# Optimization experiments

Measured on AMD Instinct MI355X. Metric: run time of the kernel, lower is better.

## Reference

```python
import jax, jax.numpy as jnp
import numpy as np


def setup_inputs() -> dict:
    key = jax.random.key(0)
    k1, k2, k3, k4 = jax.random.split(key, 4)
    B, T, C, H = 8, 2048, 1024, 64
    x = jax.random.normal(k1, (B, T, C), dtype=jnp.float32)
    Wq = jax.random.normal(k2, (C, H), dtype=jnp.float32) * (C ** -0.5)
    Wk = jax.random.normal(k3, (C, H), dtype=jnp.float32) * (C ** -0.5)
    Wv = jax.random.normal(k4, (C, H), dtype=jnp.float32) * (C ** -0.5)
    return {"x": x, "Wq": Wq, "Wk": Wk, "Wv": Wv}


def reference(x, Wq, Wk, Wv):
    # x: [B,T,C]; Wq/Wk/Wv: [C,H] (nn.Linear bias=False => x @ W)
    B, T, C = x.shape
    H = Wq.shape[-1]
    q = jnp.einsum('btc,ch->bth', x, Wq)
    k = jnp.einsum('btc,ch->bth', x, Wk)
    v = jnp.einsum('btc,ch->bth', x, Wv)
    scale = H ** -0.5
    att = jnp.einsum('bqh,bkh->bqk', q, k) * scale  # [B,T,T]
    causal = jnp.tril(jnp.ones((T, T), dtype=bool))
    att = jnp.where(causal, att, -jnp.inf)
    att = jax.nn.softmax(att, axis=-1)
    out = jnp.einsum('bqk,bkh->bqh', att, v)  # [B,T,H]
    return out
```

## Files before the change

kernel.cpp:

```cpp
#include <hip/hip_runtime.h>
#include <hip/hip_bf16.h>
#include <math.h>

#define BB 8
#define TT 2048
#define CC 1024
#define HH 64
#define BT (BB * TT)

typedef __attribute__((ext_vector_type(8))) short short8;
typedef __attribute__((ext_vector_type(4))) float floatx4;

static __device__ inline ushort f2bf(float f) {
    __hip_bfloat16 h = __float2bfloat16(f);
    return *reinterpret_cast<ushort*>(&h);
}
static __device__ inline unsigned int f2bf2(float lo, float hi) {
    __hip_bfloat162 h = __float22bfloat162_rn(make_float2(lo, hi));
    return *reinterpret_cast<unsigned int*>(&h);
}
static __device__ inline float bf2f(ushort u) {
    union { unsigned int i; float f; } c;
    c.i = ((unsigned int)u) << 16;
    return c.f;
}
static __device__ inline void gl_lds16(const ushort* g, ushort* l) {
    __builtin_amdgcn_global_load_lds(
        (const __attribute__((address_space(1))) unsigned int*)g,
        (__attribute__((address_space(3))) unsigned int*)l,
        16, 0, 0);
}

__global__ __launch_bounds__(256) void wprep_kernel(
    const float* __restrict__ Wq, const float* __restrict__ Wk,
    const float* __restrict__ Wv, ushort* __restrict__ WbT)
{
    __shared__ float ws_[128 * 65];
    const int m  = blockIdx.x >> 3;
    const int kb = (blockIdx.x & 7) * 128;
    const float* W = (m == 0) ? Wq : (m == 1) ? Wk : Wv;
    const int t  = threadIdx.x;
    const int lr = t >> 4, lc = (t & 15) * 4;
    #pragma unroll
    for (int i = 0; i < 8; ++i) {
        const int row = lr + i * 16;
        float4 v = *(const float4*)&W[(size_t)(kb + row) * HH + lc];
        ws_[row * 65 + lc + 0] = v.x; ws_[row * 65 + lc + 1] = v.y;
        ws_[row * 65 + lc + 2] = v.z; ws_[row * 65 + lc + 3] = v.w;
    }
    __syncthreads();
    const int n = t & 63, kseg = t >> 6;
    union { ushort s[32]; uint4 q[4]; } u;
    #pragma unroll
    for (int j = 0; j < 32; ++j)
        u.s[j] = f2bf(ws_[(kseg * 32 + j) * 65 + n]);
    ushort* dst = &WbT[(size_t)(m * 64 + n) * 1024 + kb + kseg * 32];
    #pragma unroll
    for (int i = 0; i < 4; ++i) *(uint4*)&dst[i * 8] = u.q[i];
}

__global__ __launch_bounds__(256) void qkv_kernel(
    const float* __restrict__ x, const ushort* __restrict__ WbT,
    ushort* __restrict__ qb, ushort* __restrict__ kbS, ushort* __restrict__ vS)
{
    __shared__ ushort As[2][256 * 8];

    const int row0 = blockIdx.x * 32;
    const int t    = threadIdx.x;
    const int w    = t >> 6;
    const int lane = t & 63;
    const int l16  = lane & 15;
    const int quad = lane >> 4;
    const int ct0  = w * 3;

    const int srow = t >> 3, sseg = t & 7;
    const int slot = (((sseg >> 2) * 2 + (srow >> 4)) * 16 + (srow & 15)) * 4 + (sseg & 3);
    const float* xsrc = &x[(size_t)(row0 + srow) * CC + sseg * 8];

    floatx4 acc[2][3];
    #pragma unroll
    for (int mt = 0; mt < 2; ++mt)
        #pragma unroll
        for (int c = 0; c < 3; ++c) acc[mt][c] = (floatx4){0.f, 0.f, 0.f, 0.f};

    float4 xa = *(const float4*)&xsrc[0];
    float4 xb = *(const float4*)&xsrc[4];

    short8 bfr[2][3];
    #pragma unroll
    for (int p = 0; p < 2; ++p)
        #pragma unroll
        for (int c = 0; c < 3; ++c)
            bfr[p][c] = *(const short8*)&WbT[(size_t)((ct0 + c) * 16 + l16) * 1024
                                             + p * 32 + quad * 8];

    #pragma unroll 2
    for (int it = 0; it < 16; ++it) {
        uint4 uq;
        uq.x = f2bf2(xa.x, xa.y); uq.y = f2bf2(xa.z, xa.w);
        uq.z = f2bf2(xb.x, xb.y); uq.w = f2bf2(xb.z, xb.w);
        *(uint4*)&As[it & 1][slot * 8] = uq;
        __syncthreads();

        if (it < 15) {
            xa = *(const float4*)&xsrc[(it + 1) * 64 + 0];
            xb = *(const float4*)&xsrc[(it + 1) * 64 + 4];
        }
        short8 bnx[2][3];
        if (it < 15) {
            const int kn = (it + 1) * 64;
            #pragma unroll
            for (int p = 0; p < 2; ++p)
                #pragma unroll
                for (int c = 0; c < 3; ++c)
                    bnx[p][c] = *(const short8*)&WbT[(size_t)((ct0 + c) * 16 + l16) * 1024
                                                     + kn + p * 32 + quad * 8];
        }

        #pragma unroll
        for (int p = 0; p < 2; ++p) {
            short8 a0 = *(const short8*)&As[it & 1][(size_t)((p * 2 + 0) * 64 + l16 * 4 + quad) * 8];
            short8 a1 = *(const short8*)&As[it & 1][(size_t)((p * 2 + 1) * 64 + l16 * 4 + quad) * 8];
            #pragma unroll
            for (int c = 0; c < 3; ++c) {
                acc[0][c] = __builtin_amdgcn_mfma_f32_16x16x32_bf16(a0, bfr[p][c], acc[0][c], 0, 0, 0);
                acc[1][c] = __builtin_amdgcn_mfma_f32_16x16x32_bf16(a1, bfr[p][c], acc[1][c], 0, 0, 0);
            }
        }
        #pragma unroll
        for (int p = 0; p < 2; ++p)
            #pragma unroll
            for (int c = 0; c < 3; ++c)
                bfr[p][c] = bnx[p][c];
    }

    const int half = (row0 >> 5) & 1;
    const size_t tile = (size_t)(row0 >> 6) * 4096;
    #pragma unroll
    for (int c = 0; c < 3; ++c) {
        const int ct    = ct0 + c;
        const int mtype = ct >> 2;
        const int n0    = (ct & 3) * 16;
        #pragma unroll
        for (int mt = 0; mt < 2; ++mt) {
            const int row = row0 + mt * 16 + quad * 4;
            if (mtype == 0) {
                #pragma unroll
                for (int reg = 0; reg < 4; ++reg)
                    qb[(size_t)(row + reg) * HH + n0 + l16] = f2bf(acc[mt][c][reg] * 0.125f);
            } else if (mtype == 1) {
                const int cP    = half * 2 + mt;
                const int pP    = (ct & 3) >> 1;
                const int quadP = ((ct & 3) * 2 + (l16 >> 3)) & 3;
                const int jP    = l16 & 7;
                const int ub    = (cP * 2 + pP) * 64 + quadP * 16;
                #pragma unroll
                for (int reg = 0; reg < 4; ++reg)
                    kbS[tile + (size_t)(ub + quad * 4 + reg) * 8 + jP] = f2bf(acc[mt][c][reg]);
            } else {
                const int cp2 = (ct & 3) * 2 + half;
                #pragma unroll
                for (int reg = 0; reg < 4; ++reg) {
                    const int rq    = quad * 4 + reg;
                    const int quadP = mt * 2 + (rq >> 3);
                    vS[tile + (size_t)(cp2 * 64 + quadP * 16 + l16) * 8 + (rq & 7)] = f2bf(acc[mt][c][reg]);
                }
            }
        }
    }
}

__global__ __launch_bounds__(256) void attn_kernel(
    const ushort* __restrict__ qb, const ushort* __restrict__ kbS,
    const ushort* __restrict__ vS, ushort* __restrict__ Opart,
    float* __restrict__ ml)
{
    __shared__ __align__(16) ushort Kb[2][4096];
    __shared__ __align__(16) ushort Vb[2][4096];
    __shared__ __align__(16) ushort P[4][16 * 72];

    const int t    = threadIdx.x;
    const int w    = t >> 6;
    const int lane = t & 63;
    const int l16  = lane & 15;
    const int quad = lane >> 4;

    const int b   = blockIdx.x & 7;
    const int idx = blockIdx.x >> 3;
    int qt, part, np;
    if (idx < 32)      { qt = 31 - (idx >> 2); part = idx & 3; np = 4; }
    else if (idx < 56) { const int u = idx - 32; const int g = u / 3;
                         qt = 23 - g; part = u - g * 3; np = 3; }
    else if (idx < 72) { const int u = idx - 56; qt = 15 - (u >> 1); part = u & 1; np = 2; }
    else               { qt = 7 - (idx - 72); part = 0; np = 1; }
    const int ntiles = qt + 1;
    const int ktb = (part * ntiles) / np;
    const int kte = ((part + 1) * ntiles) / np;

    const ushort* ktile0 = kbS + (size_t)(b * 32) * 4096;
    const ushort* vtile0 = vS  + (size_t)(b * 32) * 4096;

    short8 qf[2];
    {
        const ushort* qrow = qb + ((size_t)b * TT + qt * 64 + w * 16) * HH;
        qf[0] = *(const short8*)&qrow[l16 * HH + quad * 8];
        qf[1] = *(const short8*)&qrow[l16 * HH + 32 + quad * 8];
    }
    short8 ones;
    #pragma unroll
    for (int i = 0; i < 8; ++i) ones[i] = (short)0x3F80;

    floatx4 o[4], osum;
    #pragma unroll
    for (int c = 0; c < 4; ++c) o[c] = (floatx4){0.f, 0.f, 0.f, 0.f};
    osum = (floatx4){0.f, 0.f, 0.f, 0.f};

    {
        const ushort* gk = ktile0 + (size_t)ktb * 4096 + w * 1024 + lane * 8;
        const ushort* gv = vtile0 + (size_t)ktb * 4096 + w * 1024 + lane * 8;
        gl_lds16(gk,       &Kb[0][w * 1024]);
        gl_lds16(gk + 512, &Kb[0][w * 1024 + 512]);
        gl_lds16(gv,       &Vb[0][w * 1024]);
        gl_lds16(gv + 512, &Vb[0][w * 1024 + 512]);
    }

    ushort* Pw = &P[w][0];

    for (int kt = ktb; kt < kte; ++kt) {
        const int cur = (kt - ktb) & 1;
        __syncthreads();

        if (kt + 1 < kte) {
            const int nxt = cur ^ 1;
            const ushort* gk = ktile0 + (size_t)(kt + 1) * 4096 + w * 1024 + lane * 8;
            const ushort* gv = vtile0 + (size_t)(kt + 1) * 4096 + w * 1024 + lane * 8;
            gl_lds16(gk,       &Kb[nxt][w * 1024]);
            gl_lds16(gk + 512, &Kb[nxt][w * 1024 + 512]);
            gl_lds16(gv,       &Vb[nxt][w * 1024]);
            gl_lds16(gv + 512, &Vb[nxt][w * 1024 + 512]);
        }

        short8 kf[4][2], vf[4][2];
        #pragma unroll
        for (int c = 0; c < 4; ++c)
            #pragma unroll
            for (int p = 0; p < 2; ++p) {
                kf[c][p] = *(const short8*)&Kb[cur][(size_t)(((c * 2 + p) * 64) + lane) * 8];
                vf[c][p] = *(const short8*)&Vb[cur][(size_t)(((c * 2 + p) * 64) + lane) * 8];
            }

        floatx4 s[4];
        #pragma unroll
        for (int c = 0; c < 4; ++c) s[c] = (floatx4){0.f, 0.f, 0.f, 0.f};
        #pragma unroll
        for (int c = 0; c < 4; ++c)
            #pragma unroll
            for (int p = 0; p < 2; ++p)
                s[c] = __builtin_amdgcn_mfma_f32_16x16x32_bf16(qf[p], kf[c][p], s[c], 0, 0, 0);

        if (kt == ntiles - 1) {
            const int qrow0 = qt * 64 + w * 16 + quad * 4;
            const int key0  = kt * 64;
            #pragma unroll
            for (int c = 0; c < 4; ++c)
                #pragma unroll
                for (int reg = 0; reg < 4; ++reg)
                    if (key0 + c * 16 + l16 > qrow0 + reg) s[c][reg] = -1e30f;
        }

        #pragma unroll
        for (int c = 0; c < 4; ++c)
            #pragma unroll
            for (int reg = 0; reg < 4; ++reg)
                Pw[(quad * 4 + reg) * 72 + c * 16 + l16] = f2bf(__expf(s[c][reg]));

        short8 pf[2];
        pf[0] = *(const short8*)&Pw[l16 * 72 + quad * 8];
        pf[1] = *(const short8*)&Pw[l16 * 72 + 32 + quad * 8];

        #pragma unroll
        for (int p = 0; p < 2; ++p) {
            #pragma unroll
            for (int c = 0; c < 4; ++c)
                o[c] = __builtin_amdgcn_mfma_f32_16x16x32_bf16(pf[p], vf[c][p], o[c], 0, 0, 0);
            osum = __builtin_amdgcn_mfma_f32_16x16x32_bf16(pf[p], ones, osum, 0, 0, 0);
        }
    }

    const size_t ub = (size_t)blockIdx.x * 4096;
    #pragma unroll
    for (int c = 0; c < 4; ++c)
        #pragma unroll
        for (int reg = 0; reg < 4; ++reg)
            Opart[ub + (w * 16 + quad * 4 + reg) * 64 + c * 16 + l16] = f2bf(o[c][reg]);
    if (l16 == 0) {
        #pragma unroll
        for (int reg = 0; reg < 4; ++reg)
            ml[(size_t)blockIdx.x * 64 + w * 16 + quad * 4 + reg] = osum[reg];
    }
}

__global__ __launch_bounds__(256) void merge_kernel(
    const ushort* __restrict__ Opart, const float* __restrict__ ml,
    float* __restrict__ out)
{
    const int t    = threadIdx.x;
    const int gw   = blockIdx.x * 4 + (t >> 6);
    const int lane = t & 63;
    const int b    = gw >> 8;
    const int v    = gw & 255;
    const int qt   = v >> 3;
    const int oct  = v & 7;

    int base, np;
    if (qt >= 24)      { base = (31 - qt) * 4;      np = 4; }
    else if (qt >= 16) { base = 32 + (23 - qt) * 3; np = 3; }
    else if (qt >= 8)  { base = 56 + (15 - qt) * 2; np = 2; }
    else               { base = 72 + (7 - qt);      np = 1; }

    float* obase = out + ((size_t)b * TT + qt * 64) * HH;

    #pragma unroll 2
    for (int row = oct * 8; row < oct * 8 + 8; ++row) {
        float den = 0.f, acc = 0.f;
        for (int p = 0; p < np; ++p) {
            const int unit = (base + p) * 8 + b;
            den += ml[(size_t)unit * 64 + row];
            acc += bf2f(Opart[(size_t)unit * 4096 + row * 64 + lane]);
        }
        obase[(size_t)row * HH + lane] = acc / den;
    }
}

extern "C" void kernel_launch(void* const* d_in, const int* in_sizes, int n_in,
                              void* d_out, int out_size, void* d_ws, size_t ws_size,
                              hipStream_t stream)
{
    (void)in_sizes; (void)n_in; (void)out_size; (void)ws_size;
    const float* x  = (const float*)d_in[0];
    const float* Wq = (const float*)d_in[1];
    const float* Wk = (const float*)d_in[2];
    const float* Wv = (const float*)d_in[3];
    float* outp = (float*)d_out;

    char* base = (char*)d_ws;
    ushort* WbT   = (ushort*)(base);
    ushort* qbuf  = (ushort*)(base + 393216);
    ushort* kbS   = qbuf + (size_t)BT * HH;
    ushort* vSb   = kbS + (size_t)BT * HH;
    ushort* Opart = vSb + (size_t)BT * HH;
    float*  ml    = (float*)((char*)Opart + (size_t)640 * 4096 * 2);

    wprep_kernel<<<dim3(24),  256, 0, stream>>>(Wq, Wk, Wv, WbT);
    qkv_kernel  <<<dim3(512), 256, 0, stream>>>(x, WbT, qbuf, kbS, vSb);
    attn_kernel <<<dim3(640), 256, 0, stream>>>(qbuf, kbS, vSb, Opart, ml);
    merge_kernel<<<dim3(512), 256, 0, stream>>>(Opart, ml, outp);
}
```

Baseline: 145.7 us.

## Split weight prep finer, prefetch x two tiles ahead, vectorize merge

Three separate changes. The weight-prep kernel now uses 48 blocks of 64 rows instead of 24 blocks of 128, to spread the small transpose over more CUs. The QKV projection keeps two register sets of x loads and fetches x two iterations ahead instead of one, to hide global load latency better at the cost of more registers. The merge kernel now reads four bf16 values and writes a float4 per lane, and multiplies by a reciprocal instead of dividing per element, which cuts the number of memory instructions.

```diff
diff --git a/kernel.cpp b/kernel.cpp
--- a/kernel.cpp
+++ b/kernel.cpp
@@ -35,14 +35,14 @@
     const float* __restrict__ Wq, const float* __restrict__ Wk,
     const float* __restrict__ Wv, ushort* __restrict__ WbT)
 {
-    __shared__ float ws_[128 * 65];
-    const int m  = blockIdx.x >> 3;
-    const int kb = (blockIdx.x & 7) * 128;
+    __shared__ float ws_[64 * 65];
+    const int m  = blockIdx.x >> 4;
+    const int kb = (blockIdx.x & 15) * 64;
     const float* W = (m == 0) ? Wq : (m == 1) ? Wk : Wv;
     const int t  = threadIdx.x;
     const int lr = t >> 4, lc = (t & 15) * 4;
     #pragma unroll
-    for (int i = 0; i < 8; ++i) {
+    for (int i = 0; i < 4; ++i) {
         const int row = lr + i * 16;
         float4 v = *(const float4*)&W[(size_t)(kb + row) * HH + lc];
         ws_[row * 65 + lc + 0] = v.x; ws_[row * 65 + lc + 1] = v.y;
@@ -50,13 +50,13 @@
     }
     __syncthreads();
     const int n = t & 63, kseg = t >> 6;
-    union { ushort s[32]; uint4 q[4]; } u;
-    #pragma unroll
-    for (int j = 0; j < 32; ++j)
-        u.s[j] = f2bf(ws_[(kseg * 32 + j) * 65 + n]);
-    ushort* dst = &WbT[(size_t)(m * 64 + n) * 1024 + kb + kseg * 32];
-    #pragma unroll
-    for (int i = 0; i < 4; ++i) *(uint4*)&dst[i * 8] = u.q[i];
+    union { ushort s[16]; uint4 q[2]; } u;
+    #pragma unroll
+    for (int j = 0; j < 16; ++j)
+        u.s[j] = f2bf(ws_[(kseg * 16 + j) * 65 + n]);
+    ushort* dst = &WbT[(size_t)(m * 64 + n) * 1024 + kb + kseg * 16];
+    *(uint4*)&dst[0] = u.q[0];
+    *(uint4*)&dst[8] = u.q[1];
 }
 
 __global__ __launch_bounds__(256) void qkv_kernel(
@@ -83,8 +83,10 @@
         #pragma unroll
         for (int c = 0; c < 3; ++c) acc[mt][c] = (floatx4){0.f, 0.f, 0.f, 0.f};
 
-    float4 xa = *(const float4*)&xsrc[0];
-    float4 xb = *(const float4*)&xsrc[4];
+    float4 xa0 = *(const float4*)&xsrc[0];
+    float4 xb0 = *(const float4*)&xsrc[4];
+    float4 xa1 = *(const float4*)&xsrc[64];
+    float4 xb1 = *(const float4*)&xsrc[68];
 
     short8 bfr[2][3];
     #pragma unroll
@@ -94,17 +96,16 @@
             bfr[p][c] = *(const short8*)&WbT[(size_t)((ct0 + c) * 16 + l16) * 1024
                                              + p * 32 + quad * 8];
 
-    #pragma unroll 2
-    for (int it = 0; it < 16; ++it) {
+    auto body = [&](int it, float4& xa, float4& xb) {
         uint4 uq;
         uq.x = f2bf2(xa.x, xa.y); uq.y = f2bf2(xa.z, xa.w);
         uq.z = f2bf2(xb.x, xb.y); uq.w = f2bf2(xb.z, xb.w);
         *(uint4*)&As[it & 1][slot * 8] = uq;
         __syncthreads();
 
-        if (it < 15) {
-            xa = *(const float4*)&xsrc[(it + 1) * 64 + 0];
-            xb = *(const float4*)&xsrc[(it + 1) * 64 + 4];
+        if (it + 2 < 16) {
+            xa = *(const float4*)&xsrc[(it + 2) * 64 + 0];
+            xb = *(const float4*)&xsrc[(it + 2) * 64 + 4];
         }
         short8 bnx[2][3];
         if (it < 15) {
@@ -132,6 +133,11 @@
             #pragma unroll
             for (int c = 0; c < 3; ++c)
                 bfr[p][c] = bnx[p][c];
+    };
+
+    for (int it2 = 0; it2 < 16; it2 += 2) {
+        body(it2 + 0, xa0, xb0);
+        body(it2 + 1, xa1, xb1);
     }
 
     const int half = (row0 >> 5) & 1;
@@ -318,17 +324,25 @@
     else if (qt >= 8)  { base = 56 + (15 - qt) * 2; np = 2; }
     else               { base = 72 + (7 - qt);      np = 1; }
 
+    const int r4 = lane >> 4;
+    const int cs = (lane & 15) * 4;
     float* obase = out + ((size_t)b * TT + qt * 64) * HH;
 
-    #pragma unroll 2
-    for (int row = oct * 8; row < oct * 8 + 8; ++row) {
-        float den = 0.f, acc = 0.f;
+    #pragma unroll
+    for (int rg = 0; rg < 2; ++rg) {
+        const int row = oct * 8 + rg * 4 + r4;
+        float den = 0.f;
+        float ax = 0.f, ay = 0.f, az = 0.f, aw = 0.f;
         for (int p = 0; p < np; ++p) {
             const int unit = (base + p) * 8 + b;
             den += ml[(size_t)unit * 64 + row];
-            acc += bf2f(Opart[(size_t)unit * 4096 + row * 64 + lane]);
-        }
-        obase[(size_t)row * HH + lane] = acc / den;
+            ushort4 ov = *(const ushort4*)&Opart[(size_t)unit * 4096 + row * 64 + cs];
+            ax += bf2f(ov.x); ay += bf2f(ov.y); az += bf2f(ov.z); aw += bf2f(ov.w);
+        }
+        const float inv = 1.0f / den;
+        float4 o4;
+        o4.x = ax * inv; o4.y = ay * inv; o4.z = az * inv; o4.w = aw * inv;
+        *(float4*)&obase[(size_t)row * HH + cs] = o4;
     }
 }
 
@@ -351,7 +365,7 @@
     ushort* Opart = vSb + (size_t)BT * HH;
     float*  ml    = (float*)((char*)Opart + (size_t)640 * 4096 * 2);
 
-    wprep_kernel<<<dim3(24),  256, 0, stream>>>(Wq, Wk, Wv, WbT);
+    wprep_kernel<<<dim3(48),  256, 0, stream>>>(Wq, Wk, Wv, WbT);
     qkv_kernel  <<<dim3(512), 256, 0, stream>>>(x, WbT, qbuf, kbS, vSb);
     attn_kernel <<<dim3(640), 256, 0, stream>>>(qbuf, kbS, vSb, Opart, ml);
     merge_kernel<<<dim3(512), 256, 0, stream>>>(Opart, ml, outp);
```

Result: faster. 140.4 us (-3.6%).
